# Kernel optimization log

Measured on AMD Instinct MI355X. Metric: run time of the kernel, lower is better.

The kernel has to match this reference:

```python
import jax, jax.numpy as jnp
import numpy as np

N, E = 10000, 320000
IN, H, C, ED = 256, 4, 64, 64
HC = H * C
EPS = 1e-5
NEG_SLOPE = 0.2


def setup_inputs() -> dict:
    key = jax.random.key(0)
    ks = jax.random.split(key, 12)
    g = lambda k, shape, fan: jax.random.normal(k, shape, jnp.float32) * (1.0 / np.sqrt(fan))
    return {
        "x": jax.random.normal(ks[0], (N, IN), jnp.float32),
        "edge_index": jax.random.randint(ks[1], (2, E), 0, N, jnp.int64),
        "edge_attr": jax.random.normal(ks[2], (E, ED), jnp.float32),
        "Wl": g(ks[3], (HC, IN), IN),   # lin_l weight (source)
        "bl": jnp.zeros((HC,), jnp.float32),
        "Wr": g(ks[4], (HC, IN), IN),   # lin_r weight (target)
        "br": jnp.zeros((HC,), jnp.float32),
        "We": g(ks[5], (HC, ED), ED),   # lin_edge weight (no bias)
        "att": g(ks[6], (H, C), C),
        "bias": jnp.zeros((HC,), jnp.float32),
        "gamma": jnp.ones((HC,), jnp.float32),
        "beta": jnp.zeros((HC,), jnp.float32),
    }


def reference(x, edge_index, edge_attr, Wl, bl, Wr, br, We, att, bias, gamma, beta):
    src, dst = edge_index[0], edge_index[1]
    # add_self_loops with fill_value='mean': loop edge_attr = mean of incoming attrs
    ones = jnp.ones((E,), jnp.float32)
    cnt = jax.ops.segment_sum(ones, dst, num_segments=N)              # [N]
    loop_attr = jax.ops.segment_sum(edge_attr, dst, num_segments=N) / jnp.maximum(cnt, 1.0)[:, None]
    node_ids = jnp.arange(N, dtype=src.dtype)
    src_f = jnp.concatenate([src, node_ids])                          # [E+N]
    dst_f = jnp.concatenate([dst, node_ids])
    ea = jnp.concatenate([edge_attr, loop_attr], axis=0)              # [E+N, ED]

    xl = (x @ Wl.T + bl).reshape(N, H, C)   # source-side projection
    xr = (x @ Wr.T + br).reshape(N, H, C)   # target-side projection
    ep = (ea @ We.T).reshape(-1, H, C)       # edge projection

    m = xl[src_f] + xr[dst_f] + ep                                    # [E+N, H, C]
    m = jnp.where(m >= 0, m, NEG_SLOPE * m)                           # leaky_relu(0.2)
    logits = jnp.einsum("ehc,hc->eh", m, att)                        # [E+N, H]

    # segment softmax over target node dst_f (every node has a self loop)
    mx = jax.ops.segment_max(logits, dst_f, num_segments=N)
    ex = jnp.exp(logits - mx[dst_f])
    den = jax.ops.segment_sum(ex, dst_f, num_segments=N)
    alpha = ex / den[dst_f]                                           # [E+N, H]

    out = jax.ops.segment_sum(xl[src_f] * alpha[:, :, None], dst_f, num_segments=N)
    h = out.reshape(N, HC) + bias

    # SiLU then LayerNorm, dropout is identity in eval
    h = h * jax.nn.sigmoid(h)
    mu = jnp.mean(h, axis=-1, keepdims=True)
    var = jnp.mean((h - mu) ** 2, axis=-1, keepdims=True)
    h = (h - mu) * jax.lax.rsqrt(var + EPS) * gamma + beta
    return h, alpha
```

## Files before the change

kernel.cpp:

```cpp
#include <hip/hip_runtime.h>

#define N_NODES 10000
#define N_EDGES 320000
#define NE_TOT  330000
#define NEG_SLOPE 0.2f
#define LN_EPS 1e-5f

#define OFF_CNT    0u
#define OFF_FILL   40000u
#define OFF_ROWPTR 80128u
#define OFF_EIDS   120320u
#define OFF_LATTR  1440512u
#define OFF_XLH    4000512u
#define OFF_XRH    9120512u
#define OFF_LOG    14240512u
#define OFF_WLF    19520512u
#define OFF_WRF    19651584u
#define OFF_WEF    19782656u
#define OFF_SD     19815424u

typedef __bf16 bf16x8 __attribute__((ext_vector_type(8)));
typedef float  f32x4  __attribute__((ext_vector_type(4)));
typedef unsigned short us4 __attribute__((ext_vector_type(4)));

__device__ __forceinline__ float bf2f(unsigned short u) {
    union { unsigned int i; float f; } v;
    v.i = ((unsigned int)u) << 16;
    return v.f;
}
__device__ __forceinline__ unsigned short f2bf(float x) {
    __bf16 b = (__bf16)x;
    return __builtin_bit_cast(unsigned short, b);
}
__device__ __forceinline__ bf16x8 cvt8(const float* p) {
    float4 v0 = *reinterpret_cast<const float4*>(p);
    float4 v1 = *reinterpret_cast<const float4*>(p + 4);
    bf16x8 t;
    t[0] = (__bf16)v0.x; t[1] = (__bf16)v0.y; t[2] = (__bf16)v0.z; t[3] = (__bf16)v0.w;
    t[4] = (__bf16)v1.x; t[5] = (__bf16)v1.y; t[6] = (__bf16)v1.z; t[7] = (__bf16)v1.w;
    return t;
}

__global__ void k_count(const int* __restrict__ ei, int* __restrict__ cnt) {
    int e = blockIdx.x * blockDim.x + threadIdx.x;
    if (e < N_EDGES) atomicAdd(&cnt[ei[N_EDGES + e]], 1);
}

__global__ void k_scan(const int* __restrict__ cnt, int* __restrict__ row_ptr) {
    __shared__ int sums[1024];
    int t = threadIdx.x;
    const int CH = 10;
    int base = t * CH;
    int s = 0;
    for (int i = 0; i < CH; i++) {
        int n = base + i;
        if (n < N_NODES) s += cnt[n] + 1;
    }
    sums[t] = s;
    __syncthreads();
    for (int off = 1; off < 1024; off <<= 1) {
        int v = (t >= off) ? sums[t - off] : 0;
        __syncthreads();
        sums[t] += v;
        __syncthreads();
    }
    int run = (t == 0) ? 0 : sums[t - 1];
    for (int i = 0; i < CH; i++) {
        int n = base + i;
        if (n < N_NODES) { row_ptr[n] = run; run += cnt[n] + 1; }
    }
    if (t == 1023) row_ptr[N_NODES] = sums[1023];
}

__global__ void k_fill(const int* __restrict__ ei, const int* __restrict__ row_ptr,
                       int* __restrict__ fill, int* __restrict__ eids,
                       int* __restrict__ sdv) {
    int e = blockIdx.x * blockDim.x + threadIdx.x;
    if (e >= NE_TOT) return;
    int s, d;
    if (e < N_EDGES) { s = ei[e]; d = ei[N_EDGES + e]; }
    else             { s = e - N_EDGES; d = s; }
    int pos = atomicAdd(&fill[d], 1);
    int p = row_ptr[d] + pos;
    eids[p] = e;
    sdv[p] = s | (d << 16);
}

__global__ void k_loop_attr(const float* __restrict__ edge_attr,
                            const int* __restrict__ row_ptr,
                            const int* __restrict__ eids,
                            const int* __restrict__ cnt,
                            float* __restrict__ lattr) {
    int node = (blockIdx.x << 2) + (threadIdx.x >> 6);
    int lane = threadIdx.x & 63;
    int b = row_ptr[node], en = row_ptr[node + 1];
    float s0 = 0.0f, s1 = 0.0f, s2 = 0.0f, s3 = 0.0f;
    int i = b;
    for (; i + 3 < en; i += 4) {
        int e0 = eids[i], e1 = eids[i + 1], e2 = eids[i + 2], e3 = eids[i + 3];
        int v0 = e0 < N_EDGES, v1 = e1 < N_EDGES, v2 = e2 < N_EDGES, v3 = e3 < N_EDGES;
        float a0 = edge_attr[(size_t)(v0 ? e0 : 0) * 64 + lane];
        float a1 = edge_attr[(size_t)(v1 ? e1 : 0) * 64 + lane];
        float a2 = edge_attr[(size_t)(v2 ? e2 : 0) * 64 + lane];
        float a3 = edge_attr[(size_t)(v3 ? e3 : 0) * 64 + lane];
        s0 += v0 ? a0 : 0.0f;
        s1 += v1 ? a1 : 0.0f;
        s2 += v2 ? a2 : 0.0f;
        s3 += v3 ? a3 : 0.0f;
    }
    for (; i < en; i++) {
        int e = eids[i];
        int v = e < N_EDGES;
        float a = edge_attr[(size_t)(v ? e : 0) * 64 + lane];
        s0 += v ? a : 0.0f;
    }
    float s = (s0 + s1) + (s2 + s3);
    float c = (float)cnt[node];
    lattr[node * 64 + lane] = s / fmaxf(c, 1.0f);
}

__global__ void k_prep_wfrag(const float* __restrict__ Wl,
                             const float* __restrict__ Wr,
                             const float* __restrict__ We,
                             unsigned short* __restrict__ wlf,
                             unsigned short* __restrict__ wrf,
                             unsigned short* __restrict__ wef) {
    int idx = blockIdx.x * 256 + threadIdx.x;
    if (idx >= 8192) return;
    int ln = idx & 63;
    int ts = (idx >> 6) & 7;
    int ct = idx >> 9;
    int c = ct * 16 + (ln & 15);
    int k0 = ts * 32 + (ln >> 4) * 8;
    *reinterpret_cast<bf16x8*>(wlf + (size_t)idx * 8) = cvt8(Wl + (size_t)c * 256 + k0);
    *reinterpret_cast<bf16x8*>(wrf + (size_t)idx * 8) = cvt8(Wr + (size_t)c * 256 + k0);
    if (idx < 2048) {
        int f = idx >> 6;
        int cb = f >> 1, step = f & 1;
        int ce = cb * 16 + (ln & 15);
        int ke = step * 32 + (ln >> 4) * 8;
        *reinterpret_cast<bf16x8*>(wef + (size_t)idx * 8) = cvt8(We + (size_t)ce * 64 + ke);
    }
}

__global__ __launch_bounds__(256) void k_gemm_mfma(
        const float* __restrict__ x,
        const float* __restrict__ bl, const float* __restrict__ br,
        const unsigned short* __restrict__ wlf,
        const unsigned short* __restrict__ wrf,
        unsigned short* __restrict__ xlh,
        unsigned short* __restrict__ xrh) {
    __shared__ __bf16 xs[8 * 64 * 8];
    int tid = threadIdx.x;
    int nb = blockIdx.x * 16;

    for (int f = tid; f < 512; f += 256) {
        int t = f >> 6, ln = f & 63;
        int node = nb + (ln & 15);
        int k0 = t * 32 + (ln >> 4) * 8;
        *reinterpret_cast<bf16x8*>(&xs[f * 8]) = cvt8(x + (size_t)node * 256 + k0);
    }
    __syncthreads();

    int lane = tid & 63;
    int wv = tid >> 6;
    int quad = lane >> 4;
    int ln15 = lane & 15;

    bf16x8 bfr[8];
#pragma unroll
    for (int t = 0; t < 8; t++)
        bfr[t] = *reinterpret_cast<const bf16x8*>(&xs[(t * 64 + lane) * 8]);

    int node = nb + ln15;
#pragma unroll
    for (int ci = 0; ci < 4; ci++) {
        int ct = wv * 4 + ci;
        f32x4 accl, accr;
        accl[0] = accl[1] = accl[2] = accl[3] = 0.0f;
        accr[0] = accr[1] = accr[2] = accr[3] = 0.0f;
#pragma unroll
        for (int t = 0; t < 8; t++) {
            bf16x8 al = *reinterpret_cast<const bf16x8*>(
                wlf + ((size_t)(ct * 8 + t) * 64 + lane) * 8);
            accl = __builtin_amdgcn_mfma_f32_16x16x32_bf16(al, bfr[t], accl, 0, 0, 0);
        }
#pragma unroll
        for (int t = 0; t < 8; t++) {
            bf16x8 ar = *reinterpret_cast<const bf16x8*>(
                wrf + ((size_t)(ct * 8 + t) * 64 + lane) * 8);
            accr = __builtin_amdgcn_mfma_f32_16x16x32_bf16(ar, bfr[t], accr, 0, 0, 0);
        }
        int cbase = ct * 16 + quad * 4;
        float4 blv = *reinterpret_cast<const float4*>(bl + cbase);
        float4 brv = *reinterpret_cast<const float4*>(br + cbase);
        us4 ol, orr;
        ol[0] = f2bf(accl[0] + blv.x); ol[1] = f2bf(accl[1] + blv.y);
        ol[2] = f2bf(accl[2] + blv.z); ol[3] = f2bf(accl[3] + blv.w);
        orr[0] = f2bf(accr[0] + brv.x); orr[1] = f2bf(accr[1] + brv.y);
        orr[2] = f2bf(accr[2] + brv.z); orr[3] = f2bf(accr[3] + brv.w);
        *reinterpret_cast<us4*>(xlh + (size_t)node * 256 + cbase) = ol;
        *reinterpret_cast<us4*>(xrh + (size_t)node * 256 + cbase) = orr;
    }
}

__global__ __launch_bounds__(256) void k_logits_mfma(
        const int* __restrict__ eids,
        const int* __restrict__ sdv,
        const float* __restrict__ edge_attr,
        const float* __restrict__ lattr,
        const unsigned short* __restrict__ xlh,
        const unsigned short* __restrict__ xrh,
        const unsigned short* __restrict__ wef,
        const float* __restrict__ att,
        float* __restrict__ logits) {
    __shared__ float att_s[256];
    int tid = threadIdx.x;
    if (tid < 64) {
        reinterpret_cast<float4*>(att_s)[tid] =
            reinterpret_cast<const float4*>(att)[tid];
    }
    __syncthreads();

    int lane = tid & 63;
    int wv = tid >> 6;
    int quad = lane >> 4;
    int ln15 = lane & 15;

    const int ntiles = NE_TOT / 16;
    for (int t = blockIdx.x * 4 + wv; t < ntiles; t += gridDim.x * 4) {
        int pos = t * 16 + ln15;
        int e = eids[pos];
        int sd = sdv[pos];
        int s = sd & 0xFFFF;
        int d = sd >> 16;
        const float* row = (e < N_EDGES)
            ? edge_attr + (size_t)e * 64
            : lattr + (size_t)(e - N_EDGES) * 64;

        bf16x8 bfr[2];
#pragma unroll
        for (int step = 0; step < 2; step++)
            bfr[step] = cvt8(row + step * 32 + quad * 8);

        const unsigned short* xls = xlh + (size_t)s * 256;
        const unsigned short* xrd = xrh + (size_t)d * 256;

        float hsum[4] = {0.0f, 0.0f, 0.0f, 0.0f};
#pragma unroll 4
        for (int cb = 0; cb < 16; cb++) {
            f32x4 acc;
            acc[0] = acc[1] = acc[2] = acc[3] = 0.0f;
            bf16x8 a0 = *reinterpret_cast<const bf16x8*>(
                wef + ((size_t)(cb * 2 + 0) * 64 + lane) * 8);
            bf16x8 a1 = *reinterpret_cast<const bf16x8*>(
                wef + ((size_t)(cb * 2 + 1) * 64 + lane) * 8);
            acc = __builtin_amdgcn_mfma_f32_16x16x32_bf16(a0, bfr[0], acc, 0, 0, 0);
            acc = __builtin_amdgcn_mfma_f32_16x16x32_bf16(a1, bfr[1], acc, 0, 0, 0);

            int cbase = cb * 16 + quad * 4;
            us4 xa = *reinterpret_cast<const us4*>(xls + cbase);
            us4 xb = *reinterpret_cast<const us4*>(xrd + cbase);
            float4 at = *reinterpret_cast<const float4*>(&att_s[cbase]);
            const float* tp = reinterpret_cast<const float*>(&at);
            float hs = 0.0f;
#pragma unroll
            for (int r = 0; r < 4; r++) {
                float v = acc[r] + bf2f(xa[r]) + bf2f(xb[r]);
                v = fmaxf(v, NEG_SLOPE * v);
                hs = fmaf(v, tp[r], hs);
            }
            hsum[cb >> 2] += hs;
        }
#pragma unroll
        for (int hh = 0; hh < 4; hh++) {
            hsum[hh] += __shfl_xor(hsum[hh], 16, 64);
            hsum[hh] += __shfl_xor(hsum[hh], 32, 64);
        }
        if (quad == 0) {
            reinterpret_cast<float4*>(logits)[pos] =
                make_float4(hsum[0], hsum[1], hsum[2], hsum[3]);
        }
    }
}

__global__ void k_aggregate(const int* __restrict__ sdv,
                            const int* __restrict__ row_ptr,
                            const int* __restrict__ eids,
                            const float* __restrict__ logits,
                            const unsigned short* __restrict__ xlh,
                            const float* __restrict__ bias,
                            const float* __restrict__ gamma,
                            const float* __restrict__ beta,
                            float* __restrict__ hout,
                            float* __restrict__ alpha_out) {
    int node = (blockIdx.x << 2) + (threadIdx.x >> 6);
    int lane = threadIdx.x & 63;
    int h = lane >> 4;
    int b = row_ptr[node], en = row_ptr[node + 1];

    float m0 = -INFINITY, m1 = -INFINITY, m2 = -INFINITY, m3 = -INFINITY;
    int i = b;
    for (; i + 3 < en; i += 4) {
        m0 = fmaxf(m0, logits[(i + 0) * 4 + h]);
        m1 = fmaxf(m1, logits[(i + 1) * 4 + h]);
        m2 = fmaxf(m2, logits[(i + 2) * 4 + h]);
        m3 = fmaxf(m3, logits[(i + 3) * 4 + h]);
    }
    for (; i < en; i++) m0 = fmaxf(m0, logits[i * 4 + h]);
    float mh = fmaxf(fmaxf(m0, m1), fmaxf(m2, m3));

    float d0 = 0.0f, d1 = 0.0f, d2 = 0.0f, d3 = 0.0f;
    i = b;
    for (; i + 3 < en; i += 4) {
        d0 += __expf(logits[(i + 0) * 4 + h] - mh);
        d1 += __expf(logits[(i + 1) * 4 + h] - mh);
        d2 += __expf(logits[(i + 2) * 4 + h] - mh);
        d3 += __expf(logits[(i + 3) * 4 + h] - mh);
    }
    for (; i < en; i++) d0 += __expf(logits[i * 4 + h] - mh);
    float rden = 1.0f / ((d0 + d1) + (d2 + d3));

    int c0 = lane * 4;
    float4 ac0; ac0.x = ac0.y = ac0.z = ac0.w = 0.0f;
    float4 ac1; ac1.x = ac1.y = ac1.z = ac1.w = 0.0f;
    float4 ac2; ac2.x = ac2.y = ac2.z = ac2.w = 0.0f;
    float4 ac3; ac3.x = ac3.y = ac3.z = ac3.w = 0.0f;
    i = b;
    for (; i + 3 < en; i += 4) {
        int e0 = eids[i], e1 = eids[i + 1], e2 = eids[i + 2], e3 = eids[i + 3];
        float al0 = __expf(logits[(i + 0) * 4 + h] - mh) * rden;
        float al1 = __expf(logits[(i + 1) * 4 + h] - mh) * rden;
        float al2 = __expf(logits[(i + 2) * 4 + h] - mh) * rden;
        float al3 = __expf(logits[(i + 3) * 4 + h] - mh) * rden;
        if ((lane & 15) == 0) {
            alpha_out[e0 * 4 + h] = al0;
            alpha_out[e1 * 4 + h] = al1;
            alpha_out[e2 * 4 + h] = al2;
            alpha_out[e3 * 4 + h] = al3;
        }
        int s0 = sdv[i + 0] & 0xFFFF;
        int s1 = sdv[i + 1] & 0xFFFF;
        int s2 = sdv[i + 2] & 0xFFFF;
        int s3 = sdv[i + 3] & 0xFFFF;
        us4 x0 = *reinterpret_cast<const us4*>(xlh + (size_t)s0 * 256 + c0);
        us4 x1 = *reinterpret_cast<const us4*>(xlh + (size_t)s1 * 256 + c0);
        us4 x2 = *reinterpret_cast<const us4*>(xlh + (size_t)s2 * 256 + c0);
        us4 x3 = *reinterpret_cast<const us4*>(xlh + (size_t)s3 * 256 + c0);
        ac0.x = fmaf(al0, bf2f(x0[0]), ac0.x); ac0.y = fmaf(al0, bf2f(x0[1]), ac0.y);
        ac0.z = fmaf(al0, bf2f(x0[2]), ac0.z); ac0.w = fmaf(al0, bf2f(x0[3]), ac0.w);
        ac1.x = fmaf(al1, bf2f(x1[0]), ac1.x); ac1.y = fmaf(al1, bf2f(x1[1]), ac1.y);
        ac1.z = fmaf(al1, bf2f(x1[2]), ac1.z); ac1.w = fmaf(al1, bf2f(x1[3]), ac1.w);
        ac2.x = fmaf(al2, bf2f(x2[0]), ac2.x); ac2.y = fmaf(al2, bf2f(x2[1]), ac2.y);
        ac2.z = fmaf(al2, bf2f(x2[2]), ac2.z); ac2.w = fmaf(al2, bf2f(x2[3]), ac2.w);
        ac3.x = fmaf(al3, bf2f(x3[0]), ac3.x); ac3.y = fmaf(al3, bf2f(x3[1]), ac3.y);
        ac3.z = fmaf(al3, bf2f(x3[2]), ac3.z); ac3.w = fmaf(al3, bf2f(x3[3]), ac3.w);
    }
    for (; i < en; i++) {
        int e = eids[i];
        float al = __expf(logits[i * 4 + h] - mh) * rden;
        if ((lane & 15) == 0) alpha_out[e * 4 + h] = al;
        int s = sdv[i] & 0xFFFF;
        us4 xv = *reinterpret_cast<const us4*>(xlh + (size_t)s * 256 + c0);
        ac0.x = fmaf(al, bf2f(xv[0]), ac0.x); ac0.y = fmaf(al, bf2f(xv[1]), ac0.y);
        ac0.z = fmaf(al, bf2f(xv[2]), ac0.z); ac0.w = fmaf(al, bf2f(xv[3]), ac0.w);
    }
    float4 acc;
    acc.x = (ac0.x + ac1.x) + (ac2.x + ac3.x);
    acc.y = (ac0.y + ac1.y) + (ac2.y + ac3.y);
    acc.z = (ac0.z + ac1.z) + (ac2.z + ac3.z);
    acc.w = (ac0.w + ac1.w) + (ac2.w + ac3.w);

    const float4 b4 = reinterpret_cast<const float4*>(bias)[lane];
    float4 hv;
    hv.x = acc.x + b4.x; hv.y = acc.y + b4.y;
    hv.z = acc.z + b4.z; hv.w = acc.w + b4.w;
    hv.x = hv.x / (1.0f + __expf(-hv.x));
    hv.y = hv.y / (1.0f + __expf(-hv.y));
    hv.z = hv.z / (1.0f + __expf(-hv.z));
    hv.w = hv.w / (1.0f + __expf(-hv.w));
    float s1 = hv.x + hv.y + hv.z + hv.w;
    float s2 = hv.x * hv.x + hv.y * hv.y + hv.z * hv.z + hv.w * hv.w;
#pragma unroll
    for (int off = 1; off < 64; off <<= 1) {
        s1 += __shfl_xor(s1, off, 64);
        s2 += __shfl_xor(s2, off, 64);
    }
    float mu = s1 * (1.0f / 256.0f);
    float var = s2 * (1.0f / 256.0f) - mu * mu;
    float rs = rsqrtf(var + LN_EPS);
    const float4 g4 = reinterpret_cast<const float4*>(gamma)[lane];
    const float4 be4 = reinterpret_cast<const float4*>(beta)[lane];
    float4 o;
    o.x = (hv.x - mu) * rs * g4.x + be4.x;
    o.y = (hv.y - mu) * rs * g4.y + be4.y;
    o.z = (hv.z - mu) * rs * g4.z + be4.z;
    o.w = (hv.w - mu) * rs * g4.w + be4.w;
    reinterpret_cast<float4*>(hout)[node * 64 + lane] = o;
}

extern "C" void kernel_launch(void* const* d_in, const int* in_sizes, int n_in,
                              void* d_out, int out_size, void* d_ws, size_t ws_size,
                              hipStream_t stream) {
    (void)in_sizes; (void)n_in; (void)out_size; (void)ws_size;
    const float* x         = (const float*)d_in[0];
    const int*   ei        = (const int*)d_in[1];
    const float* edge_attr = (const float*)d_in[2];
    const float* Wl        = (const float*)d_in[3];
    const float* bl        = (const float*)d_in[4];
    const float* Wr        = (const float*)d_in[5];
    const float* br        = (const float*)d_in[6];
    const float* We        = (const float*)d_in[7];
    const float* att       = (const float*)d_in[8];
    const float* bias      = (const float*)d_in[9];
    const float* gamma     = (const float*)d_in[10];
    const float* beta      = (const float*)d_in[11];

    char* ws = (char*)d_ws;
    int*   cnt     = (int*)(ws + OFF_CNT);
    int*   fill    = (int*)(ws + OFF_FILL);
    int*   row_ptr = (int*)(ws + OFF_ROWPTR);
    int*   eids    = (int*)(ws + OFF_EIDS);
    float* lattr   = (float*)(ws + OFF_LATTR);
    unsigned short* xlh = (unsigned short*)(ws + OFF_XLH);
    unsigned short* xrh = (unsigned short*)(ws + OFF_XRH);
    float* logits  = (float*)(ws + OFF_LOG);
    unsigned short* wlf = (unsigned short*)(ws + OFF_WLF);
    unsigned short* wrf = (unsigned short*)(ws + OFF_WRF);
    unsigned short* wef = (unsigned short*)(ws + OFF_WEF);
    int*   sdv     = (int*)(ws + OFF_SD);

    float* hout      = (float*)d_out;
    float* alpha_out = (float*)d_out + N_NODES * 256;

    hipMemsetAsync(ws + OFF_CNT, 0, 2 * N_NODES * sizeof(int), stream);

    k_count<<<(N_EDGES + 255) / 256, 256, 0, stream>>>(ei, cnt);
    k_scan<<<1, 1024, 0, stream>>>(cnt, row_ptr);
    k_prep_wfrag<<<32, 256, 0, stream>>>(Wl, Wr, We, wlf, wrf, wef);
    k_fill<<<(NE_TOT + 255) / 256, 256, 0, stream>>>(ei, row_ptr, fill, eids, sdv);
    k_gemm_mfma<<<N_NODES / 16, 256, 0, stream>>>(x, bl, br, wlf, wrf, xlh, xrh);
    k_loop_attr<<<N_NODES / 4, 256, 0, stream>>>(edge_attr, row_ptr, eids, cnt, lattr);
    k_logits_mfma<<<2048, 256, 0, stream>>>(eids, sdv, edge_attr, lattr, xlh, xrh,
                                            wef, att, logits);
    k_aggregate<<<N_NODES / 4, 256, 0, stream>>>(sdv, row_ptr, eids, logits, xlh,
                                                 bias, gamma, beta, hout, alpha_out);
}
```

Baseline: 364.6 us.

## Pre-permute edge attributes into CSR order as bf16 before logits

Adds a kernel that scatters edge_attr rows into CSR (dst-sorted) order, converted to bf16, using a per-edge position array recorded during fill. The self-loop mean attribute is then computed from this contiguous bf16 buffer and written into the self-loop slot. The logits kernel reads contiguous bf16 rows instead of gathering fp32 rows through eids. This replaces random fp32 gathers with one coalesced-read scatter pass plus sequential reads, at the cost of an extra full pass over edge_attr and a bf16-rounded mean for the self-loop attribute.

Result: no change. 371.4 us (+1.9%).

```diff
diff --git a/kernel.cpp b/kernel.cpp
--- a/kernel.cpp
+++ b/kernel.cpp
@@ -10,7 +10,7 @@
 #define OFF_FILL   40000u
 #define OFF_ROWPTR 80128u
 #define OFF_EIDS   120320u
-#define OFF_LATTR  1440512u
+#define OFF_POSE   1440512u
 #define OFF_XLH    4000512u
 #define OFF_XRH    9120512u
 #define OFF_LOG    14240512u
@@ -18,6 +18,7 @@
 #define OFF_WRF    19651584u
 #define OFF_WEF    19782656u
 #define OFF_SD     19815424u
+#define OFF_EAC    21135424u
 
 typedef __bf16 bf16x8 __attribute__((ext_vector_type(8)));
 typedef float  f32x4  __attribute__((ext_vector_type(4)));
@@ -74,7 +75,7 @@
 
 __global__ void k_fill(const int* __restrict__ ei, const int* __restrict__ row_ptr,
                        int* __restrict__ fill, int* __restrict__ eids,
-                       int* __restrict__ sdv) {
+                       int* __restrict__ sdv, int* __restrict__ pose) {
     int e = blockIdx.x * blockDim.x + threadIdx.x;
     if (e >= NE_TOT) return;
     int s, d;
@@ -84,39 +85,43 @@
     int p = row_ptr[d] + pos;
     eids[p] = e;
     sdv[p] = s | (d << 16);
-}
-
-__global__ void k_loop_attr(const float* __restrict__ edge_attr,
-                            const int* __restrict__ row_ptr,
-                            const int* __restrict__ eids,
-                            const int* __restrict__ cnt,
-                            float* __restrict__ lattr) {
+    pose[e] = p;
+}
+
+__global__ void k_permute_e(const float* __restrict__ edge_attr,
+                            const int* __restrict__ pose,
+                            unsigned short* __restrict__ eac) {
+    int idx = blockIdx.x * blockDim.x + threadIdx.x;
+    if (idx >= N_EDGES * 32) return;
+    int e = idx >> 5, cp = idx & 31;
+    float2 v = reinterpret_cast<const float2*>(edge_attr)[(size_t)e * 32 + cp];
+    int p = pose[e];
+    unsigned int u = ((unsigned int)f2bf(v.x)) | (((unsigned int)f2bf(v.y)) << 16);
+    reinterpret_cast<unsigned int*>(eac)[(size_t)p * 32 + cp] = u;
+}
+
+__global__ void k_self_attr(const int* __restrict__ row_ptr,
+                            const int* __restrict__ pose,
+                            unsigned short* __restrict__ eac) {
     int node = (blockIdx.x << 2) + (threadIdx.x >> 6);
     int lane = threadIdx.x & 63;
     int b = row_ptr[node], en = row_ptr[node + 1];
-    float s0 = 0.0f, s1 = 0.0f, s2 = 0.0f, s3 = 0.0f;
+    int selfp = pose[N_EDGES + node];
+    float s0 = 0.0f, s1 = 0.0f;
     int i = b;
-    for (; i + 3 < en; i += 4) {
-        int e0 = eids[i], e1 = eids[i + 1], e2 = eids[i + 2], e3 = eids[i + 3];
-        int v0 = e0 < N_EDGES, v1 = e1 < N_EDGES, v2 = e2 < N_EDGES, v3 = e3 < N_EDGES;
-        float a0 = edge_attr[(size_t)(v0 ? e0 : 0) * 64 + lane];
-        float a1 = edge_attr[(size_t)(v1 ? e1 : 0) * 64 + lane];
-        float a2 = edge_attr[(size_t)(v2 ? e2 : 0) * 64 + lane];
-        float a3 = edge_attr[(size_t)(v3 ? e3 : 0) * 64 + lane];
-        s0 += v0 ? a0 : 0.0f;
-        s1 += v1 ? a1 : 0.0f;
-        s2 += v2 ? a2 : 0.0f;
-        s3 += v3 ? a3 : 0.0f;
+    for (; i + 1 < en; i += 2) {
+        float a0 = bf2f(eac[(size_t)(i + 0) * 64 + lane]);
+        float a1 = bf2f(eac[(size_t)(i + 1) * 64 + lane]);
+        s0 += (i + 0 == selfp) ? 0.0f : a0;
+        s1 += (i + 1 == selfp) ? 0.0f : a1;
     }
     for (; i < en; i++) {
-        int e = eids[i];
-        int v = e < N_EDGES;
-        float a = edge_attr[(size_t)(v ? e : 0) * 64 + lane];
-        s0 += v ? a : 0.0f;
-    }
-    float s = (s0 + s1) + (s2 + s3);
-    float c = (float)cnt[node];
-    lattr[node * 64 + lane] = s / fmaxf(c, 1.0f);
+        float a = bf2f(eac[(size_t)i * 64 + lane]);
+        s0 += (i == selfp) ? 0.0f : a;
+    }
+    float s = s0 + s1;
+    float c = (float)(en - b - 1);
+    eac[(size_t)selfp * 64 + lane] = f2bf(s / fmaxf(c, 1.0f));
 }
 
 __global__ void k_prep_wfrag(const float* __restrict__ Wl,
@@ -205,10 +210,8 @@
 }
 
 __global__ __launch_bounds__(256) void k_logits_mfma(
-        const int* __restrict__ eids,
         const int* __restrict__ sdv,
-        const float* __restrict__ edge_attr,
-        const float* __restrict__ lattr,
+        const unsigned short* __restrict__ eac,
         const unsigned short* __restrict__ xlh,
         const unsigned short* __restrict__ xrh,
         const unsigned short* __restrict__ wef,
@@ -230,18 +233,13 @@
     const int ntiles = NE_TOT / 16;
     for (int t = blockIdx.x * 4 + wv; t < ntiles; t += gridDim.x * 4) {
         int pos = t * 16 + ln15;
-        int e = eids[pos];
         int sd = sdv[pos];
         int s = sd & 0xFFFF;
         int d = sd >> 16;
-        const float* row = (e < N_EDGES)
-            ? edge_attr + (size_t)e * 64
-            : lattr + (size_t)(e - N_EDGES) * 64;
-
-        bf16x8 bfr[2];
-#pragma unroll
-        for (int step = 0; step < 2; step++)
-            bfr[step] = cvt8(row + step * 32 + quad * 8);
+        const unsigned short* row = eac + (size_t)pos * 64;
+
+        bf16x8 bfr0 = *reinterpret_cast<const bf16x8*>(row + quad * 8);
+        bf16x8 bfr1 = *reinterpret_cast<const bf16x8*>(row + 32 + quad * 8);
 
         const unsigned short* xls = xlh + (size_t)s * 256;
         const unsigned short* xrd = xrh + (size_t)d * 256;
@@ -255,8 +253,8 @@
                 wef + ((size_t)(cb * 2 + 0) * 64 + lane) * 8);
             bf16x8 a1 = *reinterpret_cast<const bf16x8*>(
                 wef + ((size_t)(cb * 2 + 1) * 64 + lane) * 8);
-            acc = __builtin_amdgcn_mfma_f32_16x16x32_bf16(a0, bfr[0], acc, 0, 0, 0);
-            acc = __builtin_amdgcn_mfma_f32_16x16x32_bf16(a1, bfr[1], acc, 0, 0, 0);
+            acc = __builtin_amdgcn_mfma_f32_16x16x32_bf16(a0, bfr0, acc, 0, 0, 0);
+            acc = __builtin_amdgcn_mfma_f32_16x16x32_bf16(a1, bfr1, acc, 0, 0, 0);
 
             int cbase = cb * 16 + quad * 4;
             us4 xa = *reinterpret_cast<const us4*>(xls + cbase);
@@ -421,7 +419,7 @@
     int*   fill    = (int*)(ws + OFF_FILL);
     int*   row_ptr = (int*)(ws + OFF_ROWPTR);
     int*   eids    = (int*)(ws + OFF_EIDS);
-    float* lattr   = (float*)(ws + OFF_LATTR);
+    int*   pose    = (int*)(ws + OFF_POSE);
     unsigned short* xlh = (unsigned short*)(ws + OFF_XLH);
     unsigned short* xrh = (unsigned short*)(ws + OFF_XRH);
     float* logits  = (float*)(ws + OFF_LOG);
@@ -429,6 +427,7 @@
     unsigned short* wrf = (unsigned short*)(ws + OFF_WRF);
     unsigned short* wef = (unsigned short*)(ws + OFF_WEF);
     int*   sdv     = (int*)(ws + OFF_SD);
+    unsigned short* eac = (unsigned short*)(ws + OFF_EAC);
 
     float* hout      = (float*)d_out;
     float* alpha_out = (float*)d_out + N_NODES * 256;
@@ -438,11 +437,11 @@
     k_count<<<(N_EDGES + 255) / 256, 256, 0, stream>>>(ei, cnt);
     k_scan<<<1, 1024, 0, stream>>>(cnt, row_ptr);
     k_prep_wfrag<<<32, 256, 0, stream>>>(Wl, Wr, We, wlf, wrf, wef);
-    k_fill<<<(NE_TOT + 255) / 256, 256, 0, stream>>>(ei, row_ptr, fill, eids, sdv);
+    k_fill<<<(NE_TOT + 255) / 256, 256, 0, stream>>>(ei, row_ptr, fill, eids, sdv, pose);
     k_gemm_mfma<<<N_NODES / 16, 256, 0, stream>>>(x, bl, br, wlf, wrf, xlh, xrh);
-    k_loop_attr<<<N_NODES / 4, 256, 0, stream>>>(edge_attr, row_ptr, eids, cnt, lattr);
-    k_logits_mfma<<<2048, 256, 0, stream>>>(eids, sdv, edge_attr, lattr, xlh, xrh,
-                                            wef, att, logits);
+    k_permute_e<<<(N_EDGES * 32) / 256, 256, 0, stream>>>(edge_attr, pose, eac);
+    k_self_attr<<<N_NODES / 4, 256, 0, stream>>>(row_ptr, pose, eac);
+    k_logits_mfma<<<2048, 256, 0, stream>>>(sdv, eac, xlh, xrh, wef, att, logits);
     k_aggregate<<<N_NODES / 4, 256, 0, stream>>>(sdv, row_ptr, eids, logits, xlh,
                                                  bias, gamma, beta, hout, alpha_out);
 }
```
